# Performance work log

Hardware: AMD Instinct MI355X
Metric: run time of the kernel (lower is better)

The kernel has to match this reference:

```python
import jax, jax.numpy as jnp
import numpy as np

N_NODES = 10000
N_EDGES = 320000
IN_DIM = 128
HID = 256


def setup_inputs() -> dict:
    key = jax.random.key(0)
    ks = jax.random.split(key, 10)
    s_in = 1.0 / np.sqrt(IN_DIM)
    s_h = 1.0 / np.sqrt(HID)
    return {
        "x": jax.random.normal(ks[0], (N_NODES, IN_DIM), dtype=jnp.float32),
        "edge_index": jax.random.randint(ks[1], (2, N_EDGES), 0, N_NODES, dtype=jnp.int64),
        # feature_projector Linear(IN_DIM -> HID)
        "Wp": jax.random.uniform(ks[2], (IN_DIM, HID), jnp.float32, -s_in, s_in),
        "bp": jax.random.uniform(ks[3], (HID,), jnp.float32, -s_in, s_in),
        # LSTM(input=HID, hidden=HID) params, torch layout [4H, H], gate order i,f,g,o
        "W_ih": jax.random.uniform(ks[4], (4 * HID, HID), jnp.float32, -s_h, s_h),
        "W_hh": jax.random.uniform(ks[5], (4 * HID, HID), jnp.float32, -s_h, s_h),
        "b_ih": jax.random.uniform(ks[6], (4 * HID,), jnp.float32, -s_h, s_h),
        "b_hh": jax.random.uniform(ks[7], (4 * HID,), jnp.float32, -s_h, s_h),
        # EvolveGCN-O initial weight [H, H] (glorot-style)
        "initial_weight": jax.random.normal(ks[8], (HID, HID), dtype=jnp.float32) * np.sqrt(2.0 / (2 * HID)),
        # GCNConv bias
        "b_gcn": jnp.zeros((HID,), dtype=jnp.float32),
    }


def _forward(x, edge_index, Wp, bp, W_ih, W_hh, b_ih, b_hh, initial_weight, b_gcn):
    n = x.shape[0]
    # 1) feature projection
    h = x @ Wp + bp  # [N, H]
    # 2) EvolveGCN-O: one LSTM step on the weight matrix (rows = batch),
    #    with h0 = c0 = initial_weight; evolved hidden state is the GCN weight.
    gates = initial_weight @ W_ih.T + b_ih + initial_weight @ W_hh.T + b_hh  # [H, 4H]
    i_g, f_g, g_g, o_g = jnp.split(gates, 4, axis=-1)
    c = jax.nn.sigmoid(f_g) * initial_weight + jax.nn.sigmoid(i_g) * jnp.tanh(g_g)
    W = jax.nn.sigmoid(o_g) * jnp.tanh(c)  # [H, H]
    # 3) GCN propagation with fixed W: out = D^{-1/2}(A+I)D^{-1/2} (h W) + b
    hw = h @ W  # [N, H]
    self_loop = jnp.arange(n, dtype=edge_index.dtype)
    src = jnp.concatenate([edge_index[0], self_loop])
    dst = jnp.concatenate([edge_index[1], self_loop])
    ones = jnp.ones(src.shape[0], dtype=hw.dtype)
    deg = jax.ops.segment_sum(ones, dst, num_segments=n)  # in-degree incl. self loop
    dinv = jnp.where(deg > 0, jax.lax.rsqrt(deg), 0.0)
    norm = dinv[src] * dinv[dst]  # [E+N]
    out = jax.ops.segment_sum(hw[src] * norm[:, None], dst, num_segments=n)
    return out + b_gcn


def reference(x, edge_index, Wp, bp, W_ih, W_hh, b_ih, b_hh, initial_weight, b_gcn):
    return _forward(x, edge_index, Wp, bp, W_ih, W_hh, b_ih, b_hh, initial_weight, b_gcn)
```

## Files before the change

kernel.cpp:

```cpp
#include <hip/hip_runtime.h>
#include <math.h>

#define N_NODES 10000
#define N_EDGES 320000
#define IN_DIM  128
#define HID     256
#define CAP     128

#define NB_GATES 128
#define NB_FILL  313
#define NB_XCVT  80

typedef __attribute__((ext_vector_type(8))) short frag_ab;
typedef __attribute__((ext_vector_type(4))) float frag_cd;


__device__ __forceinline__ unsigned bf16rne(float f) {
    union { float f; unsigned u; } c; c.f = f;
    return (c.u + 0x7FFFu + ((c.u >> 16) & 1u)) >> 16;
}

__global__ __launch_bounds__(256)
void k_prep(const int* __restrict__ ei, int* __restrict__ cursor,
            int* __restrict__ bucket, const float* __restrict__ iw,
            const float* __restrict__ wih, const float* __restrict__ whh,
            float* __restrict__ G, const float* __restrict__ x,
            unsigned* __restrict__ xb) {
    __shared__ float smem[6144];
    if (blockIdx.x >= NB_GATES + NB_FILL) {
        int tid = (blockIdx.x - NB_GATES - NB_FILL) * 256 + threadIdx.x;
        const float2* x2 = (const float2*)x;
        #pragma unroll
        for (int it = 0; it < 32; ++it) {
            int idx = tid + it * (NB_XCVT * 256);
            if (idx < N_NODES * 64) {
                float2 v = x2[idx];
                xb[idx] = bf16rne(v.x) | (bf16rne(v.y) << 16);
            }
        }
        return;
    }
    if (blockIdx.x >= NB_GATES) {
        int e = ((blockIdx.x - NB_GATES) * 256 + threadIdx.x) * 4;
        if (e + 3 < N_EDGES) {
            int4 s4 = *(const int4*)&ei[e];
            int4 d4 = *(const int4*)&ei[N_EDGES + e];
            int p0 = atomicAdd(&cursor[d4.x], 1);
            if (p0 < CAP) bucket[d4.x * CAP + p0] = s4.x;
            int p1 = atomicAdd(&cursor[d4.y], 1);
            if (p1 < CAP) bucket[d4.y * CAP + p1] = s4.y;
            int p2 = atomicAdd(&cursor[d4.z], 1);
            if (p2 < CAP) bucket[d4.z * CAP + p2] = s4.z;
            int p3 = atomicAdd(&cursor[d4.w], 1);
            if (p3 < CAP) bucket[d4.w * CAP + p3] = s4.w;
        } else {
            for (int q = e; q < N_EDGES; ++q) {
                int s = ei[q];
                int d = ei[N_EDGES + q];
                int pos = atomicAdd(&cursor[d], 1);
                if (pos < CAP) bucket[d * CAP + pos] = s;
            }
        }
        return;
    }
    int bid = blockIdx.x;
    int m0 = (bid & 7) * 32, n0 = (bid >> 3) * 64;
    float (*aT)[32] = (float(*)[32])smem;
    float (*bS)[64] = (float(*)[64])(smem + 2048);
    int t = threadIdx.x;
    int tm = t & 15, tn = t >> 4;
    float acc[2][4] = {};
    for (int kt = 0; kt < 4; ++kt) {
        int k0 = kt * 64;
        {
            int row = t >> 3;
            #pragma unroll
            for (int r = 0; r < 2; ++r) {
                int kq = 2 * (t & 7) + r;
                float4 av = *(const float4*)&iw[(m0 + row) * HID + k0 + 4 * kq];
                aT[4 * kq + 0][row] = av.x; aT[4 * kq + 1][row] = av.y;
                aT[4 * kq + 2][row] = av.z; aT[4 * kq + 3][row] = av.w;
            }
        }
        {
            int row = t >> 2;
            #pragma unroll
            for (int r = 0; r < 4; ++r) {
                int kq = 4 * (t & 3) + r;
                float4 b1 = *(const float4*)&wih[(n0 + row) * HID + k0 + 4 * kq];
                float4 b2 = *(const float4*)&whh[(n0 + row) * HID + k0 + 4 * kq];
                bS[4 * kq + 0][row] = b1.x + b2.x; bS[4 * kq + 1][row] = b1.y + b2.y;
                bS[4 * kq + 2][row] = b1.z + b2.z; bS[4 * kq + 3][row] = b1.w + b2.w;
            }
        }
        __syncthreads();
        #pragma unroll 8
        for (int kk = 0; kk < 64; ++kk) {
            float2 a2 = *(const float2*)&aT[kk][2 * tm];
            float4 b4 = *(const float4*)&bS[kk][4 * tn];
            float a[2] = {a2.x, a2.y};
            float b[4] = {b4.x, b4.y, b4.z, b4.w};
            #pragma unroll
            for (int i = 0; i < 2; ++i)
                #pragma unroll
                for (int j = 0; j < 4; ++j)
                    acc[i][j] = fmaf(a[i], b[j], acc[i][j]);
        }
        __syncthreads();
    }
    #pragma unroll
    for (int i = 0; i < 2; ++i) {
        float4 o = make_float4(acc[i][0], acc[i][1], acc[i][2], acc[i][3]);
        *(float4*)&G[(m0 + 2 * tm + i) * 1024 + n0 + 4 * tn] = o;
    }
}

__device__ __forceinline__ float sig_f(float x)  { return 1.f / (1.f + __expf(-x)); }
__device__ __forceinline__ float tanh_f(float x) { return 1.f - 2.f / (1.f + __expf(2.f * x)); }

__global__ __launch_bounds__(256)
void k_wev_dinv(const float* __restrict__ G, const float* __restrict__ iw,
                const float* __restrict__ b_ih, const float* __restrict__ b_hh,
                float* __restrict__ Wev, const int* __restrict__ cursor,
                float* __restrict__ dinv) {
    if (blockIdx.x >= 256) {
        int v = (blockIdx.x - 256) * 256 + threadIdx.x;
        if (v < N_NODES) dinv[v] = rsqrtf((float)(cursor[v] + 1));
        return;
    }
    int r = blockIdx.x;
    int j = threadIdx.x;
    float gi = G[r * 1024 + 0   + j] + b_ih[0   + j] + b_hh[0   + j];
    float gf = G[r * 1024 + 256 + j] + b_ih[256 + j] + b_hh[256 + j];
    float gg = G[r * 1024 + 512 + j] + b_ih[512 + j] + b_hh[512 + j];
    float go = G[r * 1024 + 768 + j] + b_ih[768 + j] + b_hh[768 + j];
    float c  = sig_f(gf) * iw[r * HID + j] + sig_f(gi) * tanh_f(gg);
    Wev[r * HID + j] = sig_f(go) * tanh_f(c);
}

__global__ __launch_bounds__(256)
void k_wc_agg(const unsigned* __restrict__ xb, const int* __restrict__ bucket,
              const int* __restrict__ cursor, const float* __restrict__ dinv,
              unsigned* __restrict__ yb, float* __restrict__ rs,
              const float* __restrict__ Wp, const float* __restrict__ bp,
              const float* __restrict__ Wev, unsigned* __restrict__ wct,
              float* __restrict__ bc) {
    __shared__ float arow[HID];
    if (blockIdx.x < 129) {
        int a = blockIdx.x;
        int j = threadIdx.x;
        const float* srcRow = (a < IN_DIM) ? &Wp[a * HID] : bp;
        arow[j] = srcRow[j];
        __syncthreads();
        float acc = 0.f;
        #pragma unroll 4
        for (int k = 0; k < HID; ++k)
            acc = fmaf(arow[k], Wev[k * HID + j], acc);
        if (a < IN_DIM)
            ((unsigned short*)wct)[j * IN_DIM + a] = (unsigned short)bf16rne(acc);
        else
            bc[j] = acc;
        return;
    }
    int wv   = threadIdx.x >> 6;
    int lane = threadIdx.x & 63;
    int v = (blockIdx.x - 129) * 4 + wv;
    int cntv = cursor[v];
    float dv = dinv[v];
    int cnt = cntv > CAP ? CAP : cntv;
    unsigned self = xb[v * 64 + lane];
    union { unsigned u; float f; } c0, c1;
    c0.u = self << 16; c1.u = self & 0xFFFF0000u;
    float acc0 = dv * c0.f, acc1 = dv * c1.f;
    float wsum = dv;
    const int4* bkt4 = (const int4*)&bucket[v * CAP];
    int j = 0;
    for (; j + 4 <= cnt; j += 4) {
        int4 s = bkt4[j >> 2];
        float w0 = dinv[s.x], w1 = dinv[s.y], w2 = dinv[s.z], w3 = dinv[s.w];
        unsigned r0 = xb[s.x * 64 + lane];
        unsigned r1 = xb[s.y * 64 + lane];
        unsigned r2 = xb[s.z * 64 + lane];
        unsigned r3 = xb[s.w * 64 + lane];
        union { unsigned u; float f; } a0, a1;
        a0.u = r0 << 16; a1.u = r0 & 0xFFFF0000u;
        acc0 = fmaf(w0, a0.f, acc0); acc1 = fmaf(w0, a1.f, acc1);
        a0.u = r1 << 16; a1.u = r1 & 0xFFFF0000u;
        acc0 = fmaf(w1, a0.f, acc0); acc1 = fmaf(w1, a1.f, acc1);
        a0.u = r2 << 16; a1.u = r2 & 0xFFFF0000u;
        acc0 = fmaf(w2, a0.f, acc0); acc1 = fmaf(w2, a1.f, acc1);
        a0.u = r3 << 16; a1.u = r3 & 0xFFFF0000u;
        acc0 = fmaf(w3, a0.f, acc0); acc1 = fmaf(w3, a1.f, acc1);
        wsum += w0 + w1 + w2 + w3;
    }
    for (; j < cnt; ++j) {
        int s = ((const int*)bkt4)[j];
        float w = dinv[s];
        unsigned r = xb[s * 64 + lane];
        union { unsigned u; float f; } a0, a1;
        a0.u = r << 16; a1.u = r & 0xFFFF0000u;
        acc0 = fmaf(w, a0.f, acc0); acc1 = fmaf(w, a1.f, acc1);
        wsum += w;
    }
    yb[v * 64 + lane] = bf16rne(dv * acc0) | (bf16rne(dv * acc1) << 16);
    if (lane == 0) rs[v] = dv * wsum;
}

__global__ __launch_bounds__(256)
void k_out(const unsigned* __restrict__ yb, const unsigned* __restrict__ wct,
           const float* __restrict__ bc, const float* __restrict__ rs,
           const float* __restrict__ b_gcn, float* __restrict__ out) {
    int m0 = blockIdx.x * 16;
    int w = threadIdx.x >> 6, lane = threadIdx.x & 63;
    int q = lane >> 4, ln = lane & 15;
    const int4* yb4  = (const int4*)yb;
    const int4* wct4 = (const int4*)wct;
    union { int4 v; frag_ab f; } a[4];
    #pragma unroll
    for (int kc = 0; kc < 4; ++kc)
        a[kc].v = yb4[(m0 + ln) * 16 + kc * 4 + q];
    float rsv[4];
    #pragma unroll
    for (int r = 0; r < 4; ++r) rsv[r] = rs[m0 + q * 4 + r];
    #pragma unroll
    for (int i = 0; i < 4; ++i) {
        int n0 = (w + 4 * i) * 16;
        union { int4 v; frag_ab f; } b[4];
        #pragma unroll
        for (int kc = 0; kc < 4; ++kc)
            b[kc].v = wct4[(n0 + ln) * 16 + kc * 4 + q];
        frag_cd acc = {0.f, 0.f, 0.f, 0.f};
        #pragma unroll
        for (int kc = 0; kc < 4; ++kc)
            acc = __builtin_amdgcn_mfma_f32_16x16x32_bf16(a[kc].f, b[kc].f, acc, 0, 0, 0);
        int n = n0 + ln;
        float bcv = bc[n], bgv = b_gcn[n];
        #pragma unroll
        for (int r = 0; r < 4; ++r) {
            int m = m0 + q * 4 + r;
            out[m * HID + n] = acc[r] + rsv[r] * bcv + bgv;
        }
    }
}

extern "C" void kernel_launch(void* const* d_in, const int* in_sizes, int n_in,
                              void* d_out, int out_size, void* d_ws, size_t ws_size,
                              hipStream_t stream) {
    const float* x     = (const float*)d_in[0];
    const int*   ei    = (const int*)d_in[1];
    const float* Wp    = (const float*)d_in[2];
    const float* bp    = (const float*)d_in[3];
    const float* W_ih  = (const float*)d_in[4];
    const float* W_hh  = (const float*)d_in[5];
    const float* b_ih  = (const float*)d_in[6];
    const float* b_hh  = (const float*)d_in[7];
    const float* iw    = (const float*)d_in[8];
    const float* b_gcn = (const float*)d_in[9];
    float* out = (float*)d_out;

    char* ws = (char*)d_ws;
    unsigned* yb     = (unsigned*)(ws + 0);
    float*    G      = (float*)   (ws + 2560000);
    float*    Wev    = (float*)   (ws + 3608576);
    unsigned* wct    = (unsigned*)(ws + 3870720);
    float*    bc     = (float*)   (ws + 3936256);
    float*    rs     = (float*)   (ws + 3937280);
    unsigned* xb     = (unsigned*)(ws + 3977280);
    int*      cursor = (int*)     (ws + 6537280);
    float*    dinv   = (float*)   (ws + 6577280);
    int*      bucket = (int*)     (ws + 6617280);

    hipMemsetAsync(cursor, 0, N_NODES * sizeof(int), stream);

    k_prep<<<NB_GATES + NB_FILL + NB_XCVT, 256, 0, stream>>>(
        ei, cursor, bucket, iw, W_ih, W_hh, G, x, xb);
    k_wev_dinv<<<256 + 40, 256, 0, stream>>>(G, iw, b_ih, b_hh, Wev, cursor, dinv);
    k_wc_agg<<<129 + 2500, 256, 0, stream>>>(xb, bucket, cursor, dinv, yb, rs, Wp, bp, Wev, wct, bc);
    k_out<<<625, 256, 0, stream>>>(yb, wct, bc, rs, b_gcn, out);
}
```

Before: 136.5 us.

## Prescale features by dinv at bf16 conversion and stage output tiles through LDS

The x-to-bf16 conversion moves into the kernel that runs after degree counting, so each source row can be prescaled by its dinv. That turns the per-edge FMA in aggregation into a plain add and drops the dinv weight from the hot loop (the dinv load stays for the row-sum term). The output GEMM now does 32 rows per block with two MFMA tiles sharing each B fragment, writes results to LDS, and emits float4 coalesced stores. This adds LDS use and a barrier, rounds the prescaled values to bf16 slightly differently, and can only start the conversion after the cursor counts exist.

```diff
diff --git a/kernel.cpp b/kernel.cpp
--- a/kernel.cpp
+++ b/kernel.cpp
@@ -24,22 +24,8 @@
 void k_prep(const int* __restrict__ ei, int* __restrict__ cursor,
             int* __restrict__ bucket, const float* __restrict__ iw,
             const float* __restrict__ wih, const float* __restrict__ whh,
-            float* __restrict__ G, const float* __restrict__ x,
-            unsigned* __restrict__ xb) {
+            float* __restrict__ G) {
     __shared__ float smem[6144];
-    if (blockIdx.x >= NB_GATES + NB_FILL) {
-        int tid = (blockIdx.x - NB_GATES - NB_FILL) * 256 + threadIdx.x;
-        const float2* x2 = (const float2*)x;
-        #pragma unroll
-        for (int it = 0; it < 32; ++it) {
-            int idx = tid + it * (NB_XCVT * 256);
-            if (idx < N_NODES * 64) {
-                float2 v = x2[idx];
-                xb[idx] = bf16rne(v.x) | (bf16rne(v.y) << 16);
-            }
-        }
-        return;
-    }
     if (blockIdx.x >= NB_GATES) {
         int e = ((blockIdx.x - NB_GATES) * 256 + threadIdx.x) * 4;
         if (e + 3 < N_EDGES) {
@@ -119,10 +105,26 @@
 __device__ __forceinline__ float tanh_f(float x) { return 1.f - 2.f / (1.f + __expf(2.f * x)); }
 
 __global__ __launch_bounds__(256)
-void k_wev_dinv(const float* __restrict__ G, const float* __restrict__ iw,
-                const float* __restrict__ b_ih, const float* __restrict__ b_hh,
-                float* __restrict__ Wev, const int* __restrict__ cursor,
-                float* __restrict__ dinv) {
+void k_wev_dinv_xcvt(const float* __restrict__ G, const float* __restrict__ iw,
+                     const float* __restrict__ b_ih, const float* __restrict__ b_hh,
+                     float* __restrict__ Wev, const int* __restrict__ cursor,
+                     float* __restrict__ dinv, const float* __restrict__ x,
+                     unsigned* __restrict__ xb) {
+    if (blockIdx.x >= 296) {
+        int tid = (blockIdx.x - 296) * 256 + threadIdx.x;
+        const float2* x2 = (const float2*)x;
+        #pragma unroll
+        for (int it = 0; it < 32; ++it) {
+            int idx = tid + it * (NB_XCVT * 256);
+            if (idx < N_NODES * 64) {
+                int v = idx >> 6;
+                float dv = rsqrtf((float)(cursor[v] + 1));
+                float2 val = x2[idx];
+                xb[idx] = bf16rne(dv * val.x) | (bf16rne(dv * val.y) << 16);
+            }
+        }
+        return;
+    }
     if (blockIdx.x >= 256) {
         int v = (blockIdx.x - 256) * 256 + threadIdx.x;
         if (v < N_NODES) dinv[v] = rsqrtf((float)(cursor[v] + 1));
@@ -171,7 +173,7 @@
     unsigned self = xb[v * 64 + lane];
     union { unsigned u; float f; } c0, c1;
     c0.u = self << 16; c1.u = self & 0xFFFF0000u;
-    float acc0 = dv * c0.f, acc1 = dv * c1.f;
+    float acc0 = c0.f, acc1 = c1.f;
     float wsum = dv;
     const int4* bkt4 = (const int4*)&bucket[v * CAP];
     int j = 0;
@@ -183,24 +185,18 @@
         unsigned r2 = xb[s.z * 64 + lane];
         unsigned r3 = xb[s.w * 64 + lane];
         union { unsigned u; float f; } a0, a1;
-        a0.u = r0 << 16; a1.u = r0 & 0xFFFF0000u;
-        acc0 = fmaf(w0, a0.f, acc0); acc1 = fmaf(w0, a1.f, acc1);
-        a0.u = r1 << 16; a1.u = r1 & 0xFFFF0000u;
-        acc0 = fmaf(w1, a0.f, acc0); acc1 = fmaf(w1, a1.f, acc1);
-        a0.u = r2 << 16; a1.u = r2 & 0xFFFF0000u;
-        acc0 = fmaf(w2, a0.f, acc0); acc1 = fmaf(w2, a1.f, acc1);
-        a0.u = r3 << 16; a1.u = r3 & 0xFFFF0000u;
-        acc0 = fmaf(w3, a0.f, acc0); acc1 = fmaf(w3, a1.f, acc1);
+        a0.u = r0 << 16; a1.u = r0 & 0xFFFF0000u; acc0 += a0.f; acc1 += a1.f;
+        a0.u = r1 << 16; a1.u = r1 & 0xFFFF0000u; acc0 += a0.f; acc1 += a1.f;
+        a0.u = r2 << 16; a1.u = r2 & 0xFFFF0000u; acc0 += a0.f; acc1 += a1.f;
+        a0.u = r3 << 16; a1.u = r3 & 0xFFFF0000u; acc0 += a0.f; acc1 += a1.f;
         wsum += w0 + w1 + w2 + w3;
     }
     for (; j < cnt; ++j) {
         int s = ((const int*)bkt4)[j];
-        float w = dinv[s];
+        wsum += dinv[s];
         unsigned r = xb[s * 64 + lane];
         union { unsigned u; float f; } a0, a1;
-        a0.u = r << 16; a1.u = r & 0xFFFF0000u;
-        acc0 = fmaf(w, a0.f, acc0); acc1 = fmaf(w, a1.f, acc1);
-        wsum += w;
+        a0.u = r << 16; a1.u = r & 0xFFFF0000u; acc0 += a0.f; acc1 += a1.f;
     }
     yb[v * 64 + lane] = bf16rne(dv * acc0) | (bf16rne(dv * acc1) << 16);
     if (lane == 0) rs[v] = dv * wsum;
@@ -210,35 +206,57 @@
 void k_out(const unsigned* __restrict__ yb, const unsigned* __restrict__ wct,
            const float* __restrict__ bc, const float* __restrict__ rs,
            const float* __restrict__ b_gcn, float* __restrict__ out) {
-    int m0 = blockIdx.x * 16;
+    __shared__ float sm[32][260];
+    int m0 = blockIdx.x * 32;
     int w = threadIdx.x >> 6, lane = threadIdx.x & 63;
     int q = lane >> 4, ln = lane & 15;
     const int4* yb4  = (const int4*)yb;
     const int4* wct4 = (const int4*)wct;
-    union { int4 v; frag_ab f; } a[4];
+    union F { int4 v; frag_ab f; };
+    F a[2][4];
     #pragma unroll
-    for (int kc = 0; kc < 4; ++kc)
-        a[kc].v = yb4[(m0 + ln) * 16 + kc * 4 + q];
-    float rsv[4];
-    #pragma unroll
-    for (int r = 0; r < 4; ++r) rsv[r] = rs[m0 + q * 4 + r];
+    for (int mt = 0; mt < 2; ++mt)
+        #pragma unroll
+        for (int kc = 0; kc < 4; ++kc)
+            a[mt][kc].v = yb4[(m0 + mt * 16 + ln) * 16 + kc * 4 + q];
     #pragma unroll
     for (int i = 0; i < 4; ++i) {
-        int n0 = (w + 4 * i) * 16;
-        union { int4 v; frag_ab f; } b[4];
+        int n0w = w * 64 + i * 16;
+        F b[4];
         #pragma unroll
         for (int kc = 0; kc < 4; ++kc)
-            b[kc].v = wct4[(n0 + ln) * 16 + kc * 4 + q];
-        frag_cd acc = {0.f, 0.f, 0.f, 0.f};
-        #pragma unroll
-        for (int kc = 0; kc < 4; ++kc)
-            acc = __builtin_amdgcn_mfma_f32_16x16x32_bf16(a[kc].f, b[kc].f, acc, 0, 0, 0);
-        int n = n0 + ln;
-        float bcv = bc[n], bgv = b_gcn[n];
+            b[kc].v = wct4[(n0w + ln) * 16 + kc * 4 + q];
+        frag_cd acc0 = {0.f, 0.f, 0.f, 0.f};
+        frag_cd acc1 = {0.f, 0.f, 0.f, 0.f};
+        #pragma unroll
+        for (int kc = 0; kc < 4; ++kc) {
+            acc0 = __builtin_amdgcn_mfma_f32_16x16x32_bf16(a[0][kc].f, b[kc].f, acc0, 0, 0, 0);
+            acc1 = __builtin_amdgcn_mfma_f32_16x16x32_bf16(a[1][kc].f, b[kc].f, acc1, 0, 0, 0);
+        }
         #pragma unroll
         for (int r = 0; r < 4; ++r) {
-            int m = m0 + q * 4 + r;
-            out[m * HID + n] = acc[r] + rsv[r] * bcv + bgv;
+            sm[q * 4 + r][n0w + ln]      = acc0[r];
+            sm[16 + q * 4 + r][n0w + ln] = acc1[r];
+        }
+    }
+    __syncthreads();
+    int m  = threadIdx.x >> 3;
+    int cg = threadIdx.x & 7;
+    int gm = m0 + m;
+    if (gm < N_NODES) {
+        float rsv = rs[gm];
+        #pragma unroll
+        for (int c = 0; c < 8; ++c) {
+            int col = c * 32 + cg * 4;
+            float4 vv  = *(float4*)&sm[m][col];
+            float4 bcv = *(const float4*)&bc[col];
+            float4 bgv = *(const float4*)&b_gcn[col];
+            float4 o;
+            o.x = vv.x + rsv * bcv.x + bgv.x;
+            o.y = vv.y + rsv * bcv.y + bgv.y;
+            o.z = vv.z + rsv * bcv.z + bgv.z;
+            o.w = vv.w + rsv * bcv.w + bgv.w;
+            *(float4*)&out[gm * HID + col] = o;
         }
     }
 }
@@ -272,9 +290,9 @@
 
     hipMemsetAsync(cursor, 0, N_NODES * sizeof(int), stream);
 
-    k_prep<<<NB_GATES + NB_FILL + NB_XCVT, 256, 0, stream>>>(
-        ei, cursor, bucket, iw, W_ih, W_hh, G, x, xb);
-    k_wev_dinv<<<256 + 40, 256, 0, stream>>>(G, iw, b_ih, b_hh, Wev, cursor, dinv);
+    k_prep<<<NB_GATES + NB_FILL, 256, 0, stream>>>(ei, cursor, bucket, iw, W_ih, W_hh, G);
+    k_wev_dinv_xcvt<<<256 + 40 + NB_XCVT, 256, 0, stream>>>(
+        G, iw, b_ih, b_hh, Wev, cursor, dinv, x, xb);
     k_wc_agg<<<129 + 2500, 256, 0, stream>>>(xb, bucket, cursor, dinv, yb, rs, Wp, bp, Wev, wct, bc);
-    k_out<<<625, 256, 0, stream>>>(yb, wct, bc, rs, b_gcn, out);
-}
+    k_out<<<313, 256, 0, stream>>>(yb, wct, bc, rs, b_gcn, out);
+}
```

Result: slower. 143.7 us (+5.3%).
